# Performance work log

Measured on AMD Instinct MI355X. Metric: run time of the kernel, lower is better.

## Reference

```python
import jax, jax.numpy as jnp
import numpy as np

INPUT_SIZE, HIDDEN_SIZE, OUTPUT_SIZE, NUM_LAYERS = 64, 128, 32, 2
B, T = 256, 1024


def setup_inputs() -> dict:
    key = jax.random.key(0)
    ks = jax.random.split(key, 12)
    s = 1.0 / np.sqrt(HIDDEN_SIZE)  # PyTorch LSTM init range
    x = jax.random.normal(ks[0], (B, T, INPUT_SIZE), dtype=jnp.float32)
    h0 = jnp.zeros((NUM_LAYERS, B, HIDDEN_SIZE), dtype=jnp.float32)
    c0 = jnp.zeros((NUM_LAYERS, B, HIDDEN_SIZE), dtype=jnp.float32)
    # layer 0: input -> hidden; layer 1: hidden -> hidden. Gate order i,f,g,o (PyTorch).
    W_ih0 = jax.random.uniform(ks[1], (4 * HIDDEN_SIZE, INPUT_SIZE), minval=-s, maxval=s)
    W_hh0 = jax.random.uniform(ks[2], (4 * HIDDEN_SIZE, HIDDEN_SIZE), minval=-s, maxval=s)
    b_ih0 = jax.random.uniform(ks[3], (4 * HIDDEN_SIZE,), minval=-s, maxval=s)
    b_hh0 = jax.random.uniform(ks[4], (4 * HIDDEN_SIZE,), minval=-s, maxval=s)
    W_ih1 = jax.random.uniform(ks[5], (4 * HIDDEN_SIZE, HIDDEN_SIZE), minval=-s, maxval=s)
    W_hh1 = jax.random.uniform(ks[6], (4 * HIDDEN_SIZE, HIDDEN_SIZE), minval=-s, maxval=s)
    b_ih1 = jax.random.uniform(ks[7], (4 * HIDDEN_SIZE,), minval=-s, maxval=s)
    b_hh1 = jax.random.uniform(ks[8], (4 * HIDDEN_SIZE,), minval=-s, maxval=s)
    fc_w = jax.random.uniform(ks[9], (OUTPUT_SIZE, HIDDEN_SIZE), minval=-s, maxval=s)
    fc_b = jax.random.uniform(ks[10], (OUTPUT_SIZE,), minval=-s, maxval=s)
    return dict(x=x, h0=h0, c0=c0,
                W_ih0=W_ih0, W_hh0=W_hh0, b_ih0=b_ih0, b_hh0=b_hh0,
                W_ih1=W_ih1, W_hh1=W_hh1, b_ih1=b_ih1, b_hh1=b_hh1,
                fc_w=fc_w, fc_b=fc_b)


def _lstm_layer(x_btf, h0, c0, W_ih, W_hh, b_ih, b_hh):
    """x_btf: [B,T,F] -> (out [B,T,H], hT [B,H], cT [B,H]). PyTorch gate order i,f,g,o."""
    H = h0.shape[-1]
    # Precompute input contribution for all timesteps as one big GEMM.
    xp = jnp.einsum('btf,gf->btg', x_btf, W_ih) + b_ih + b_hh  # [B,T,4H]
    xp = jnp.swapaxes(xp, 0, 1)  # time-major [T,B,4H]

    def step(carry, xp_t):
        h, c = carry
        gates = xp_t + h @ W_hh.T  # [B,4H]
        i = jax.nn.sigmoid(gates[:, 0 * H:1 * H])
        f = jax.nn.sigmoid(gates[:, 1 * H:2 * H])
        g = jnp.tanh(gates[:, 2 * H:3 * H])
        o = jax.nn.sigmoid(gates[:, 3 * H:4 * H])
        c = f * c + i * g
        h = o * jnp.tanh(c)
        return (h, c), h

    (hT, cT), hs = jax.lax.scan(step, (h0, c0), xp)
    return jnp.swapaxes(hs, 0, 1), hT, cT  # back to batch_first


def reference(x, h0, c0, W_ih0, W_hh0, b_ih0, b_hh0,
              W_ih1, W_hh1, b_ih1, b_hh1, fc_w, fc_b):
    out0, h_0, c_0 = _lstm_layer(x, h0[0], c0[0], W_ih0, W_hh0, b_ih0, b_hh0)
    out1, h_1, c_1 = _lstm_layer(out0, h0[1], c0[1], W_ih1, W_hh1, b_ih1, b_hh1)
    out = jnp.einsum('bth,oh->bto', out1, fc_w) + fc_b  # [B,T,output_size]
    hN = jnp.stack([h_0, h_1])  # [num_layers,B,H]
    cN = jnp.stack([c_0, c_1])
    return out, hN, cN
```

## Files before the change

### kernel.cpp

```cpp
#include <hip/hip_runtime.h>


static constexpr int B   = 256;
static constexpr int T   = 1024;
static constexpr int H   = 128;
static constexpr int O   = 32;
static constexpr int R   = 4;
static constexpr int NBL = B / R;
static constexpr int CH  = 16;
static constexpr int NCH = T / CH;

typedef __attribute__((ext_vector_type(8))) short  short8;
typedef __attribute__((ext_vector_type(4))) float  f32x4;

#define LOG2E 1.4426950408889634f

#if __has_builtin(__builtin_amdgcn_exp2f)
#define EXP2(x) __builtin_amdgcn_exp2f(x)
#else
#define EXP2(x) __expf((x) * 0.69314718056f)
#endif
#if __has_builtin(__builtin_amdgcn_rcpf)
#define RCP(x) __builtin_amdgcn_rcpf(x)
#else
#define RCP(x) (1.0f / (x))
#endif

__device__ __forceinline__ unsigned short f2bf(float f) {
  unsigned int u = __builtin_bit_cast(unsigned int, f);
  u += 0x7fffu + ((u >> 16) & 1u);
  return (unsigned short)(u >> 16);
}

__device__ __forceinline__ float sigm(float x) {
  return RCP(1.0f + EXP2(-LOG2E * x));
}
__device__ __forceinline__ float tanh_f(float x) {
  return 1.0f - 2.0f * RCP(1.0f + EXP2(2.0f * LOG2E * x));
}

__device__ __forceinline__ void block_sync_lds() {
  __builtin_amdgcn_sched_barrier(0);
  asm volatile("s_waitcnt lgkmcnt(0)" ::: "memory");
  __builtin_amdgcn_s_barrier();
  __builtin_amdgcn_sched_barrier(0);
}

template <int KIN, bool IN_BF16, bool WRITE_HOUT, bool FUSE_FC, bool PROD, bool CONS>
__device__ __forceinline__ void scan_body(
    unsigned short* __restrict__ Ash,
    const void* __restrict__ in_,
    const float* __restrict__ h0,
    const float* __restrict__ c0,
    const float* __restrict__ Wih,
    const float* __restrict__ Whh,
    const float* __restrict__ bih,
    const float* __restrict__ bhh,
    unsigned short* __restrict__ hout,
    float* __restrict__ hN,
    float* __restrict__ cN,
    const float* __restrict__ Wfc,
    const float* __restrict__ bfc,
    float* __restrict__ fco,
    int* __restrict__ flag, const int bbase)
{
  constexpr int AK   = KIN + H;
  constexpr int KCX  = KIN / 32;
  constexpr int KCH  = H / 32;
  constexpr int APAD = AK + 8;

  const int tid  = threadIdx.x;
  const int w    = tid >> 6;
  const int l    = tid & 63;
  const int l15  = l & 15;
  const int lhi  = l >> 4;
  const int jcol = w * 16 + l15;

#define AEL(buf, row, col) Ash[(((buf) * 16 + (row)) * APAD) + (col)]

  short8 wfx[4][KCX], wfh[4][KCH];
  float  bias4[4];
#pragma unroll
  for (int gb = 0; gb < 4; ++gb) {
    const int gc = gb * H + jcol;
    const float* wi = Wih + (size_t)gc * KIN;
    const float* wh = Whh + (size_t)gc * H;
#pragma unroll
    for (int kc = 0; kc < KCX; ++kc) {
      const float* s = wi + kc * 32 + lhi * 8;
      float4 a = *(const float4*)s;
      float4 b = *(const float4*)(s + 4);
      short8 v;
      v[0] = (short)f2bf(a.x); v[1] = (short)f2bf(a.y);
      v[2] = (short)f2bf(a.z); v[3] = (short)f2bf(a.w);
      v[4] = (short)f2bf(b.x); v[5] = (short)f2bf(b.y);
      v[6] = (short)f2bf(b.z); v[7] = (short)f2bf(b.w);
      wfx[gb][kc] = v;
    }
#pragma unroll
    for (int kc = 0; kc < KCH; ++kc) {
      const float* s = wh + kc * 32 + lhi * 8;
      float4 a = *(const float4*)s;
      float4 b = *(const float4*)(s + 4);
      short8 v;
      v[0] = (short)f2bf(a.x); v[1] = (short)f2bf(a.y);
      v[2] = (short)f2bf(a.z); v[3] = (short)f2bf(a.w);
      v[4] = (short)f2bf(b.x); v[5] = (short)f2bf(b.y);
      v[6] = (short)f2bf(b.z); v[7] = (short)f2bf(b.w);
      wfh[gb][kc] = v;
    }
    bias4[gb] = bih[gc] + bhh[gc];
  }

  short8 bfr[4];
  float fcbias = 0.f;
  if constexpr (FUSE_FC) {
    const int oc = (w & 1) * 16 + l15;
#pragma unroll
    for (int kc = 0; kc < 4; ++kc) {
      const float* s = Wfc + (size_t)oc * H + kc * 32 + lhi * 8;
      float4 a = *(const float4*)s;
      float4 b = *(const float4*)(s + 4);
      short8 v;
      v[0] = (short)f2bf(a.x); v[1] = (short)f2bf(a.y);
      v[2] = (short)f2bf(a.z); v[3] = (short)f2bf(a.w);
      v[4] = (short)f2bf(b.x); v[5] = (short)f2bf(b.y);
      v[6] = (short)f2bf(b.z); v[7] = (short)f2bf(b.w);
      bfr[kc] = v;
    }
    fcbias = bfc[oc];
  }

  float cst   = c0[(size_t)(bbase + lhi) * H + jcol];
  float hlast = 0.f;

  const float*          inf = (const float*)in_;
  const unsigned short* inb = (const unsigned short*)in_;

  const bool sact = tid < 128;
  const int  srow = (tid >> 5) & 3;
  int scol;
  if constexpr (!IN_BF16) scol = (tid * 2) & 63;
  else                    scol = (tid * 4) & 127;
  const int srm = srow * 4;
  const float*          xpf = inf + (size_t)(bbase + srow) * T * KIN + scol;
  const unsigned short* xpb = inb + (size_t)(bbase + srow) * T * KIN + scol;

  unsigned short* hp = nullptr;
  if constexpr (WRITE_HOUT)
    hp = hout + (size_t)(bbase + lhi) * T * H + jcol;
  float* fp = nullptr;
  if constexpr (FUSE_FC)
    fp = fco + (size_t)(bbase + lhi) * T * O + (w & 1) * 16 + l15;

  for (int i = tid; i < 16 * APAD; i += 512)
    ((unsigned int*)Ash)[i] = 0u;
  __syncthreads();

  if constexpr (CONS) {
    if (tid == 0) {
      while (__hip_atomic_load(flag, __ATOMIC_ACQUIRE, __HIP_MEMORY_SCOPE_AGENT) < 2)
        __builtin_amdgcn_s_sleep(4);
    }
    __syncthreads();
  }

  if (sact) {
    if constexpr (!IN_BF16) {
      float2 v0 = *(const float2*)xpf;
      float2 v1 = *(const float2*)(xpf + KIN);
      *(unsigned int*)&AEL(1, srm, scol) =
          (unsigned int)f2bf(v0.x) | ((unsigned int)f2bf(v0.y) << 16);
      *(unsigned int*)&AEL(0, srm, scol) =
          (unsigned int)f2bf(v1.x) | ((unsigned int)f2bf(v1.y) << 16);
    } else {
      uint2 v0 = *(const uint2*)xpb;
      uint2 v1 = *(const uint2*)(xpb + KIN);
      *(uint2*)&AEL(1, srm, scol) = v0;
      *(uint2*)&AEL(0, srm, scol) = v1;
    }
  }
  if (tid < 128) {
    const int row = tid >> 5, col = (tid * 4) & 127;
    float4 v = *(const float4*)(h0 + (size_t)(bbase + row) * H + col);
    uint2 p;
    p.x = (unsigned int)f2bf(v.x) | ((unsigned int)f2bf(v.y) << 16);
    p.y = (unsigned int)f2bf(v.z) | ((unsigned int)f2bf(v.w) << 16);
    *(uint2*)&AEL(0, row * 4, KIN + col) = p;
  }

  float2 pfoF = {0.f, 0.f}; uint2 pfoB = {0u, 0u};
  if (sact) {
    if constexpr (!IN_BF16) pfoF = *(const float2*)(xpf + 2 * (size_t)KIN);
    else                    pfoB = *(const uint2*)(xpb + 2 * (size_t)KIN);
  }
  xpf += 3 * (size_t)KIN;
  xpb += 3 * (size_t)KIN;
  __syncthreads();

  f32x4 accX[4];
  {
    short8 afx[KCX];
#pragma unroll
    for (int kc = 0; kc < KCX; ++kc)
      afx[kc] = *(const short8*)&AEL(1, l15, kc * 32 + lhi * 8);
#pragma unroll
    for (int gb = 0; gb < 4; ++gb) {
      f32x4 a = {bias4[gb], bias4[gb], bias4[gb], bias4[gb]};
#pragma unroll
      for (int kc = 0; kc < KCX; ++kc)
        a = __builtin_amdgcn_mfma_f32_16x16x32_bf16(afx[kc], wfx[gb][kc], a, 0, 0, 0);
      accX[gb] = a;
    }
  }
  __syncthreads();

  int cur = 0;
  for (int k = 0; k < NCH; ++k) {
    if constexpr (CONS) {
      if (k > 0) {
        const int want = (k + 2 > NCH) ? NCH : (k + 2);
        if (tid == 0) {
          while (__hip_atomic_load(flag, __ATOMIC_ACQUIRE, __HIP_MEMORY_SCOPE_AGENT) < want)
            __builtin_amdgcn_s_sleep(4);
        }
        __syncthreads();
      }
    }

    for (int tt = 0; tt < CH; ++tt) {
      const int t   = k * CH + tt;
      const int nxt = cur ^ 1;

      float2 pfnF = {0.f, 0.f}; uint2 pfnB = {0u, 0u};
      if (sact) {
        if constexpr (!IN_BF16) {
          pfnF = *(const float2*)xpf;
          *(unsigned int*)&AEL(nxt, srm, scol) =
              (unsigned int)f2bf(pfoF.x) | ((unsigned int)f2bf(pfoF.y) << 16);
        } else {
          pfnB = *(const uint2*)xpb;
          *(uint2*)&AEL(nxt, srm, scol) = pfoB;
        }
      }

      short8 afh[KCH];
#pragma unroll
      for (int kc = 0; kc < KCH; ++kc)
        afh[kc] = *(const short8*)&AEL(cur, l15, KIN + kc * 32 + lhi * 8);
      short8 afx[KCX];
#pragma unroll
      for (int kc = 0; kc < KCX; ++kc)
        afx[kc] = *(const short8*)&AEL(cur, l15, kc * 32 + lhi * 8);

      f32x4 acc[4];
#pragma unroll
      for (int gb = 0; gb < 4; ++gb) {
        f32x4 a = accX[gb];
#pragma unroll
        for (int kc = 0; kc < KCH; ++kc)
          a = __builtin_amdgcn_mfma_f32_16x16x32_bf16(afh[kc], wfh[gb][kc], a, 0, 0, 0);
        acc[gb] = a;
      }

      f32x4 fs = {fcbias, fcbias, fcbias, fcbias};
      if constexpr (FUSE_FC) {
        if (w < 2 && t > 0) {
#pragma unroll
          for (int kc = 0; kc < 4; ++kc)
            fs = __builtin_amdgcn_mfma_f32_16x16x32_bf16(afh[kc], bfr[kc], fs, 0, 0, 0);
        }
      }

      {
        float i_ = sigm(acc[0][0]);
        float f_ = sigm(acc[1][0]);
        float g_ = tanh_f(acc[2][0]);
        float o_ = sigm(acc[3][0]);
        float c_ = f_ * cst + i_ * g_;
        cst = c_;
        float hn = o_ * tanh_f(c_);
        hlast = hn;
        unsigned short hb = f2bf(hn);
        AEL(nxt, lhi * 4, KIN + jcol) = hb;
        if constexpr (WRITE_HOUT) { hp[0] = hb; }
      }
      if constexpr (WRITE_HOUT) hp += H;

      if constexpr (FUSE_FC) {
        if (w < 2 && t > 0)
          fp[(size_t)(t - 1) * O] = fs[0];
      }

#pragma unroll
      for (int gb = 0; gb < 4; ++gb) {
        f32x4 a = {bias4[gb], bias4[gb], bias4[gb], bias4[gb]};
#pragma unroll
        for (int kc = 0; kc < KCX; ++kc)
          a = __builtin_amdgcn_mfma_f32_16x16x32_bf16(afx[kc], wfx[gb][kc], a, 0, 0, 0);
        accX[gb] = a;
      }

      block_sync_lds();
      cur = nxt;
      if constexpr (!IN_BF16) pfoF = pfnF; else pfoB = pfnB;
      if (t <= T - 5) { xpf += KIN; xpb += KIN; }
    }

    if constexpr (PROD) {
      __builtin_amdgcn_sched_barrier(0);
      asm volatile("s_waitcnt vmcnt(0)" ::: "memory");
      __builtin_amdgcn_s_barrier();
      if (tid == 0)
        __hip_atomic_store(flag, k + 1, __ATOMIC_RELEASE, __HIP_MEMORY_SCOPE_AGENT);
    }
  }

  {
    const size_t b = bbase + lhi;
    hN[b * H + jcol] = hlast;
    cN[b * H + jcol] = cst;
  }
  if constexpr (FUSE_FC) {
    if (w < 2) {
      short8 a4[4];
#pragma unroll
      for (int kc = 0; kc < 4; ++kc)
        a4[kc] = *(const short8*)&AEL(cur, l15, KIN + kc * 32 + lhi * 8);
      f32x4 fs = {fcbias, fcbias, fcbias, fcbias};
#pragma unroll
      for (int kc = 0; kc < 4; ++kc)
        fs = __builtin_amdgcn_mfma_f32_16x16x32_bf16(a4[kc], bfr[kc], fs, 0, 0, 0);
      fp[(size_t)(T - 1) * O] = fs[0];
    }
  }
#undef AEL
}

__global__ __launch_bounds__(512, 2) void lstm_fused(
    const float* __restrict__ x,
    const float* __restrict__ h0, const float* __restrict__ c0,
    const float* __restrict__ Wih0, const float* __restrict__ Whh0,
    const float* __restrict__ bih0, const float* __restrict__ bhh0,
    const float* __restrict__ Wih1, const float* __restrict__ Whh1,
    const float* __restrict__ bih1, const float* __restrict__ bhh1,
    const float* __restrict__ fcw, const float* __restrict__ fcb,
    unsigned short* __restrict__ out0,
    float* __restrict__ out, float* __restrict__ hN, float* __restrict__ cN,
    int* __restrict__ flags)
{
  __shared__ __align__(16) unsigned short Ash[2 * 16 * 264];
  const int bid = blockIdx.x;
  if (bid < NBL) {
    scan_body<64, false, true, false, true, false>(
        Ash, x, h0, c0, Wih0, Whh0, bih0, bhh0,
        out0, hN, cN, nullptr, nullptr, nullptr,
        flags + bid, bid * R);
  } else {
    const int rb = bid - NBL;
    scan_body<128, true, false, true, false, true>(
        Ash, out0, h0 + B * H, c0 + B * H, Wih1, Whh1, bih1, bhh1,
        nullptr, hN + B * H, cN + B * H, fcw, fcb, out,
        flags + rb, rb * R);
  }
}

extern "C" void kernel_launch(void* const* d_in, const int* in_sizes, int n_in,
                              void* d_out, int out_size, void* d_ws, size_t ws_size,
                              hipStream_t stream) {
  (void)in_sizes; (void)n_in; (void)out_size; (void)ws_size;

  const float* x    = (const float*)d_in[0];
  const float* h0   = (const float*)d_in[1];
  const float* c0   = (const float*)d_in[2];
  const float* Wih0 = (const float*)d_in[3];
  const float* Whh0 = (const float*)d_in[4];
  const float* bih0 = (const float*)d_in[5];
  const float* bhh0 = (const float*)d_in[6];
  const float* Wih1 = (const float*)d_in[7];
  const float* Whh1 = (const float*)d_in[8];
  const float* bih1 = (const float*)d_in[9];
  const float* bhh1 = (const float*)d_in[10];
  const float* fcw  = (const float*)d_in[11];
  const float* fcb  = (const float*)d_in[12];

  int*            flags = (int*)d_ws;
  unsigned short* out0  = (unsigned short*)((char*)d_ws + 1024);

  float* out = (float*)d_out;
  float* hN  = out + (size_t)B * T * O;
  float* cN  = hN + (size_t)2 * B * H;

  hipMemsetAsync(d_ws, 0, 1024, stream);
  lstm_fused<<<2 * NBL, 512, 0, stream>>>(
      x, h0, c0, Wih0, Whh0, bih0, bhh0, Wih1, Whh1, bih1, bhh1,
      fcw, fcb, out0, out, hN, cN, flags);
}
```

Measured before the change: 766.2 us.

## Load x operand fragments directly from global into registers, shrink LDS to h only

The per-step input rows no longer go through LDS. Each lane loads its MFMA A-fragment for x straight from global memory, two steps ahead; lanes that do not hold a real batch row read from a zeroed pad in the workspace. LDS now holds only the bf16 hidden state, stored in a pre-swizzled fragment layout so each lane reads it with one contiguous short8 per k-chunk. The x-projection MFMAs move earlier in the step, before the gate math. This removes LDS write/read traffic and bank-conflicted strided reads from the serial recurrence, at the cost of more global loads and registers per lane.

Measured after the change: 825.8 us. 1.08x slower.

```diff
diff --git a/kernel.cpp b/kernel.cpp
--- a/kernel.cpp
+++ b/kernel.cpp
@@ -62,12 +62,12 @@
     const float* __restrict__ Wfc,
     const float* __restrict__ bfc,
     float* __restrict__ fco,
+    const void* __restrict__ zpad,
     int* __restrict__ flag, const int bbase)
 {
-  constexpr int AK   = KIN + H;
   constexpr int KCX  = KIN / 32;
   constexpr int KCH  = H / 32;
-  constexpr int APAD = AK + 8;
+  constexpr int HBUF = KCH * 512;
 
   const int tid  = threadIdx.x;
   const int w    = tid >> 6;
@@ -75,8 +75,6 @@
   const int l15  = l & 15;
   const int lhi  = l >> 4;
   const int jcol = w * 16 + l15;
-
-#define AEL(buf, row, col) Ash[(((buf) * 16 + (row)) * APAD) + (col)]
 
   short8 wfx[4][KCX], wfh[4][KCH];
   float  bias4[4];
@@ -134,17 +132,23 @@
   float cst   = c0[(size_t)(bbase + lhi) * H + jcol];
   float hlast = 0.f;
 
-  const float*          inf = (const float*)in_;
-  const unsigned short* inb = (const unsigned short*)in_;
-
-  const bool sact = tid < 128;
-  const int  srow = (tid >> 5) & 3;
-  int scol;
-  if constexpr (!IN_BF16) scol = (tid * 2) & 63;
-  else                    scol = (tid * 4) & 127;
-  const int srm = srow * 4;
-  const float*          xpf = inf + (size_t)(bbase + srow) * T * KIN + scol;
-  const unsigned short* xpb = inb + (size_t)(bbase + srow) * T * KIN + scol;
+  const int hws = (jcol >> 5) * 512 +
+                  (lhi * 4 + 16 * ((w & 1) * 2 + (l15 >> 3))) * 8 + (jcol & 7);
+
+  const bool xact = (l15 & 3) == 0;
+  const int  br   = l15 >> 2;
+  const float*          xf = nullptr;
+  const unsigned short* xb = nullptr;
+  size_t xstep;
+  if constexpr (!IN_BF16) {
+    xf = xact ? ((const float*)in_ + (size_t)(bbase + br) * T * KIN + lhi * 8)
+              : (const float*)zpad;
+    xstep = xact ? (size_t)KIN : 0;
+  } else {
+    xb = xact ? ((const unsigned short*)in_ + (size_t)(bbase + br) * T * KIN + lhi * 8)
+              : (const unsigned short*)zpad;
+    xstep = xact ? (size_t)KIN : 0;
+  }
 
   unsigned short* hp = nullptr;
   if constexpr (WRITE_HOUT)
@@ -153,7 +157,7 @@
   if constexpr (FUSE_FC)
     fp = fco + (size_t)(bbase + lhi) * T * O + (w & 1) * 16 + l15;
 
-  for (int i = tid; i < 16 * APAD; i += 512)
+  for (int i = tid; i < HBUF; i += 512)
     ((unsigned int*)Ash)[i] = 0u;
   __syncthreads();
 
@@ -165,51 +169,57 @@
     __syncthreads();
   }
 
-  if (sact) {
-    if constexpr (!IN_BF16) {
-      float2 v0 = *(const float2*)xpf;
-      float2 v1 = *(const float2*)(xpf + KIN);
-      *(unsigned int*)&AEL(1, srm, scol) =
-          (unsigned int)f2bf(v0.x) | ((unsigned int)f2bf(v0.y) << 16);
-      *(unsigned int*)&AEL(0, srm, scol) =
-          (unsigned int)f2bf(v1.x) | ((unsigned int)f2bf(v1.y) << 16);
-    } else {
-      uint2 v0 = *(const uint2*)xpb;
-      uint2 v1 = *(const uint2*)(xpb + KIN);
-      *(uint2*)&AEL(1, srm, scol) = v0;
-      *(uint2*)&AEL(0, srm, scol) = v1;
-    }
-  }
-  if (tid < 128) {
-    const int row = tid >> 5, col = (tid * 4) & 127;
-    float4 v = *(const float4*)(h0 + (size_t)(bbase + row) * H + col);
-    uint2 p;
-    p.x = (unsigned int)f2bf(v.x) | ((unsigned int)f2bf(v.y) << 16);
-    p.y = (unsigned int)f2bf(v.z) | ((unsigned int)f2bf(v.w) << 16);
-    *(uint2*)&AEL(0, row * 4, KIN + col) = p;
-  }
-
-  float2 pfoF = {0.f, 0.f}; uint2 pfoB = {0u, 0u};
-  if (sact) {
-    if constexpr (!IN_BF16) pfoF = *(const float2*)(xpf + 2 * (size_t)KIN);
-    else                    pfoB = *(const uint2*)(xpb + 2 * (size_t)KIN);
-  }
-  xpf += 3 * (size_t)KIN;
-  xpb += 3 * (size_t)KIN;
-  __syncthreads();
+  Ash[hws] = f2bf(h0[(size_t)(bbase + lhi) * H + jcol]);
 
   f32x4 accX[4];
-  {
-    short8 afx[KCX];
-#pragma unroll
-    for (int kc = 0; kc < KCX; ++kc)
-      afx[kc] = *(const short8*)&AEL(1, l15, kc * 32 + lhi * 8);
+  float4 xcF[2 * KCX]; short8 xcB[KCX];
+  if constexpr (!IN_BF16) {
+    float4 x0[2 * KCX];
+#pragma unroll
+    for (int kc = 0; kc < KCX; ++kc) {
+      x0[2 * kc]     = *(const float4*)(xf + kc * 32);
+      x0[2 * kc + 1] = *(const float4*)(xf + kc * 32 + 4);
+    }
+    xf += xstep;
+#pragma unroll
+    for (int kc = 0; kc < KCX; ++kc) {
+      xcF[2 * kc]     = *(const float4*)(xf + kc * 32);
+      xcF[2 * kc + 1] = *(const float4*)(xf + kc * 32 + 4);
+    }
+    xf += xstep;
+    short8 fr[KCX];
+#pragma unroll
+    for (int kc = 0; kc < KCX; ++kc) {
+      float4 a = x0[2 * kc], b = x0[2 * kc + 1];
+      short8 v;
+      v[0] = (short)f2bf(a.x); v[1] = (short)f2bf(a.y);
+      v[2] = (short)f2bf(a.z); v[3] = (short)f2bf(a.w);
+      v[4] = (short)f2bf(b.x); v[5] = (short)f2bf(b.y);
+      v[6] = (short)f2bf(b.z); v[7] = (short)f2bf(b.w);
+      fr[kc] = v;
+    }
 #pragma unroll
     for (int gb = 0; gb < 4; ++gb) {
       f32x4 a = {bias4[gb], bias4[gb], bias4[gb], bias4[gb]};
 #pragma unroll
       for (int kc = 0; kc < KCX; ++kc)
-        a = __builtin_amdgcn_mfma_f32_16x16x32_bf16(afx[kc], wfx[gb][kc], a, 0, 0, 0);
+        a = __builtin_amdgcn_mfma_f32_16x16x32_bf16(fr[kc], wfx[gb][kc], a, 0, 0, 0);
+      accX[gb] = a;
+    }
+  } else {
+    short8 x0[KCX];
+#pragma unroll
+    for (int kc = 0; kc < KCX; ++kc) x0[kc] = *(const short8*)(xb + kc * 32);
+    xb += xstep;
+#pragma unroll
+    for (int kc = 0; kc < KCX; ++kc) xcB[kc] = *(const short8*)(xb + kc * 32);
+    xb += xstep;
+#pragma unroll
+    for (int gb = 0; gb < 4; ++gb) {
+      f32x4 a = {bias4[gb], bias4[gb], bias4[gb], bias4[gb]};
+#pragma unroll
+      for (int kc = 0; kc < KCX; ++kc)
+        a = __builtin_amdgcn_mfma_f32_16x16x32_bf16(x0[kc], wfx[gb][kc], a, 0, 0, 0);
       accX[gb] = a;
     }
   }
@@ -232,26 +242,22 @@
       const int t   = k * CH + tt;
       const int nxt = cur ^ 1;
 
-      float2 pfnF = {0.f, 0.f}; uint2 pfnB = {0u, 0u};
-      if (sact) {
-        if constexpr (!IN_BF16) {
-          pfnF = *(const float2*)xpf;
-          *(unsigned int*)&AEL(nxt, srm, scol) =
-              (unsigned int)f2bf(pfoF.x) | ((unsigned int)f2bf(pfoF.y) << 16);
-        } else {
-          pfnB = *(const uint2*)xpb;
-          *(uint2*)&AEL(nxt, srm, scol) = pfoB;
-        }
+      float4 xnF[2 * KCX]; short8 xnB[KCX];
+      if constexpr (!IN_BF16) {
+#pragma unroll
+        for (int kc = 0; kc < KCX; ++kc) {
+          xnF[2 * kc]     = *(const float4*)(xf + kc * 32);
+          xnF[2 * kc + 1] = *(const float4*)(xf + kc * 32 + 4);
+        }
+      } else {
+#pragma unroll
+        for (int kc = 0; kc < KCX; ++kc) xnB[kc] = *(const short8*)(xb + kc * 32);
       }
 
       short8 afh[KCH];
 #pragma unroll
       for (int kc = 0; kc < KCH; ++kc)
-        afh[kc] = *(const short8*)&AEL(cur, l15, KIN + kc * 32 + lhi * 8);
-      short8 afx[KCX];
-#pragma unroll
-      for (int kc = 0; kc < KCX; ++kc)
-        afx[kc] = *(const short8*)&AEL(cur, l15, kc * 32 + lhi * 8);
+        afh[kc] = *(const short8*)&Ash[cur * HBUF + kc * 512 + l * 8];
 
       f32x4 acc[4];
 #pragma unroll
@@ -269,6 +275,37 @@
 #pragma unroll
           for (int kc = 0; kc < 4; ++kc)
             fs = __builtin_amdgcn_mfma_f32_16x16x32_bf16(afh[kc], bfr[kc], fs, 0, 0, 0);
+        }
+      }
+
+      if constexpr (!IN_BF16) {
+        short8 fr[KCX];
+#pragma unroll
+        for (int kc = 0; kc < KCX; ++kc) {
+          float4 a = xcF[2 * kc], b = xcF[2 * kc + 1];
+          short8 v;
+          v[0] = (short)f2bf(a.x); v[1] = (short)f2bf(a.y);
+          v[2] = (short)f2bf(a.z); v[3] = (short)f2bf(a.w);
+          v[4] = (short)f2bf(b.x); v[5] = (short)f2bf(b.y);
+          v[6] = (short)f2bf(b.z); v[7] = (short)f2bf(b.w);
+          fr[kc] = v;
+        }
+#pragma unroll
+        for (int gb = 0; gb < 4; ++gb) {
+          f32x4 a = {bias4[gb], bias4[gb], bias4[gb], bias4[gb]};
+#pragma unroll
+          for (int kc = 0; kc < KCX; ++kc)
+            a = __builtin_amdgcn_mfma_f32_16x16x32_bf16(fr[kc], wfx[gb][kc], a, 0, 0, 0);
+          accX[gb] = a;
+        }
+      } else {
+#pragma unroll
+        for (int gb = 0; gb < 4; ++gb) {
+          f32x4 a = {bias4[gb], bias4[gb], bias4[gb], bias4[gb]};
+#pragma unroll
+          for (int kc = 0; kc < KCX; ++kc)
+            a = __builtin_amdgcn_mfma_f32_16x16x32_bf16(xcB[kc], wfx[gb][kc], a, 0, 0, 0);
+          accX[gb] = a;
         }
       }
 
@@ -282,7 +319,7 @@
         float hn = o_ * tanh_f(c_);
         hlast = hn;
         unsigned short hb = f2bf(hn);
-        AEL(nxt, lhi * 4, KIN + jcol) = hb;
+        Ash[nxt * HBUF + hws] = hb;
         if constexpr (WRITE_HOUT) { hp[0] = hb; }
       }
       if constexpr (WRITE_HOUT) hp += H;
@@ -292,19 +329,18 @@
           fp[(size_t)(t - 1) * O] = fs[0];
       }
 
-#pragma unroll
-      for (int gb = 0; gb < 4; ++gb) {
-        f32x4 a = {bias4[gb], bias4[gb], bias4[gb], bias4[gb]};
-#pragma unroll
-        for (int kc = 0; kc < KCX; ++kc)
-          a = __builtin_amdgcn_mfma_f32_16x16x32_bf16(afx[kc], wfx[gb][kc], a, 0, 0, 0);
-        accX[gb] = a;
+      if constexpr (!IN_BF16) {
+#pragma unroll
+        for (int q = 0; q < 2 * KCX; ++q) xcF[q] = xnF[q];
+        if (t <= T - 4) xf += xstep;
+      } else {
+#pragma unroll
+        for (int q = 0; q < KCX; ++q) xcB[q] = xnB[q];
+        if (t <= T - 4) xb += xstep;
       }
 
       block_sync_lds();
       cur = nxt;
-      if constexpr (!IN_BF16) pfoF = pfnF; else pfoB = pfnB;
-      if (t <= T - 5) { xpf += KIN; xpb += KIN; }
     }
 
     if constexpr (PROD) {
@@ -326,7 +362,7 @@
       short8 a4[4];
 #pragma unroll
       for (int kc = 0; kc < 4; ++kc)
-        a4[kc] = *(const short8*)&AEL(cur, l15, KIN + kc * 32 + lhi * 8);
+        a4[kc] = *(const short8*)&Ash[cur * HBUF + kc * 512 + l * 8];
       f32x4 fs = {fcbias, fcbias, fcbias, fcbias};
 #pragma unroll
       for (int kc = 0; kc < 4; ++kc)
@@ -334,7 +370,6 @@
       fp[(size_t)(T - 1) * O] = fs[0];
     }
   }
-#undef AEL
 }
 
 __global__ __launch_bounds__(512, 2) void lstm_fused(
@@ -347,20 +382,20 @@
     const float* __restrict__ fcw, const float* __restrict__ fcb,
     unsigned short* __restrict__ out0,
     float* __restrict__ out, float* __restrict__ hN, float* __restrict__ cN,
-    int* __restrict__ flags)
+    int* __restrict__ flags, const void* __restrict__ zpad)
 {
-  __shared__ __align__(16) unsigned short Ash[2 * 16 * 264];
+  __shared__ __align__(16) unsigned short Ash[2 * 2048];
   const int bid = blockIdx.x;
   if (bid < NBL) {
     scan_body<64, false, true, false, true, false>(
         Ash, x, h0, c0, Wih0, Whh0, bih0, bhh0,
-        out0, hN, cN, nullptr, nullptr, nullptr,
+        out0, hN, cN, nullptr, nullptr, nullptr, zpad,
         flags + bid, bid * R);
   } else {
     const int rb = bid - NBL;
     scan_body<128, true, false, true, false, true>(
         Ash, out0, h0 + B * H, c0 + B * H, Wih1, Whh1, bih1, bhh1,
-        nullptr, hN + B * H, cN + B * H, fcw, fcb, out,
+        nullptr, hN + B * H, cN + B * H, fcw, fcb, out, zpad,
         flags + rb, rb * R);
   }
 }
@@ -385,6 +420,7 @@
   const float* fcb  = (const float*)d_in[12];
 
   int*            flags = (int*)d_ws;
+  const void*     zpad  = (const void*)((char*)d_ws + 512);
   unsigned short* out0  = (unsigned short*)((char*)d_ws + 1024);
 
   float* out = (float*)d_out;
@@ -394,5 +430,5 @@
   hipMemsetAsync(d_ws, 0, 1024, stream);
   lstm_fused<<<2 * NBL, 512, 0, stream>>>(
       x, h0, c0, Wih0, Whh0, bih0, bhh0, Wih1, Whh1, bih1, bhh1,
-      fcw, fcb, out0, out, hN, cN, flags);
-}
+      fcw, fcb, out0, out, hN, cN, flags, zpad);
+}
```

## Batch input projection and FC per time chunk outside the recurrent loop

Applied to the files above, without the earlier changes.

The input-to-gate MFMA now runs once per chunk of 8 timesteps, packing 4 batch rows × 8 timesteps into full 16-row tiles. The results are stored to LDS as bf16 and read back at each step. The FC head is likewise computed once per chunk from buffered hidden states instead of per step, and the chunk size drops from 16 to 8. This takes the input GEMM and FC MFMAs off the serial per-step critical path and uses otherwise wasted tile rows, at the cost of more LDS traffic and bf16 rounding of the precomputed gate inputs.

After: 713.8 us. 6.8% less time.

```diff
diff --git a/kernel.cpp b/kernel.cpp
--- a/kernel.cpp
+++ b/kernel.cpp
@@ -7,8 +7,16 @@
 static constexpr int O   = 32;
 static constexpr int R   = 4;
 static constexpr int NBL = B / R;
-static constexpr int CH  = 16;
+static constexpr int CH  = 8;
 static constexpr int NCH = T / CH;
+
+static constexpr int HROW = H + 8;
+static constexpr int HB   = 0;
+static constexpr int HH   = HB + 2 * 16 * HROW;
+static constexpr int XB   = HH + 2 * 16 * HROW;
+static constexpr int AX   = XB + 2 * 16 * HROW;
+static constexpr int AXB  = 8 * 520 + 8;
+static constexpr int LDSN = AX + 4 * AXB;
 
 typedef __attribute__((ext_vector_type(8))) short  short8;
 typedef __attribute__((ext_vector_type(4))) float  f32x4;
@@ -31,6 +39,9 @@
   u += 0x7fffu + ((u >> 16) & 1u);
   return (unsigned short)(u >> 16);
 }
+__device__ __forceinline__ float bf2f(unsigned short s) {
+  return __builtin_bit_cast(float, (unsigned int)s << 16);
+}
 
 __device__ __forceinline__ float sigm(float x) {
   return RCP(1.0f + EXP2(-LOG2E * x));
@@ -48,7 +59,7 @@
 
 template <int KIN, bool IN_BF16, bool WRITE_HOUT, bool FUSE_FC, bool PROD, bool CONS>
 __device__ __forceinline__ void scan_body(
-    unsigned short* __restrict__ Ash,
+    unsigned short* __restrict__ S,
     const void* __restrict__ in_,
     const float* __restrict__ h0,
     const float* __restrict__ c0,
@@ -64,10 +75,9 @@
     float* __restrict__ fco,
     int* __restrict__ flag, const int bbase)
 {
-  constexpr int AK   = KIN + H;
   constexpr int KCX  = KIN / 32;
   constexpr int KCH  = H / 32;
-  constexpr int APAD = AK + 8;
+  constexpr int XROW = KIN + 8;
 
   const int tid  = threadIdx.x;
   const int w    = tid >> 6;
@@ -75,8 +85,6 @@
   const int l15  = l & 15;
   const int lhi  = l >> 4;
   const int jcol = w * 16 + l15;
-
-#define AEL(buf, row, col) Ash[(((buf) * 16 + (row)) * APAD) + (col)]
 
   short8 wfx[4][KCX], wfh[4][KCH];
   float  bias4[4];
@@ -137,24 +145,21 @@
   const float*          inf = (const float*)in_;
   const unsigned short* inb = (const unsigned short*)in_;
 
-  const bool sact = tid < 128;
-  const int  srow = (tid >> 5) & 3;
-  int scol;
-  if constexpr (!IN_BF16) scol = (tid * 2) & 63;
-  else                    scol = (tid * 4) & 127;
-  const int srm = srow * 4;
-  const float*          xpf = inf + (size_t)(bbase + srow) * T * KIN + scol;
-  const unsigned short* xpb = inb + (size_t)(bbase + srow) * T * KIN + scol;
+  const int sq  = tid >> 8;
+  const int srw = (tid >> 4) & 15;
+  const int sb  = bbase + sq * 2 + (srw >> 3);
+  const int sts = srw & 7;
+  const float*          xsf = inf + ((size_t)sb * T + sts) * KIN + (tid & 15) * 4;
+  const unsigned short* xsb = inb + ((size_t)sb * T + sts) * KIN + (tid & 15) * 8;
+  const int xdst = XB + (sq * 16 + srw) * XROW +
+                   (IN_BF16 ? (tid & 15) * 8 : (tid & 15) * 4);
 
   unsigned short* hp = nullptr;
   if constexpr (WRITE_HOUT)
     hp = hout + (size_t)(bbase + lhi) * T * H + jcol;
-  float* fp = nullptr;
-  if constexpr (FUSE_FC)
-    fp = fco + (size_t)(bbase + lhi) * T * O + (w & 1) * 16 + l15;
-
-  for (int i = tid; i < 16 * APAD; i += 512)
-    ((unsigned int*)Ash)[i] = 0u;
+
+  for (int i = tid; i < 2 * 16 * HROW / 2; i += 512)
+    ((unsigned int*)S)[i] = 0u;
   __syncthreads();
 
   if constexpr (CONS) {
@@ -165,54 +170,17 @@
     __syncthreads();
   }
 
-  if (sact) {
-    if constexpr (!IN_BF16) {
-      float2 v0 = *(const float2*)xpf;
-      float2 v1 = *(const float2*)(xpf + KIN);
-      *(unsigned int*)&AEL(1, srm, scol) =
-          (unsigned int)f2bf(v0.x) | ((unsigned int)f2bf(v0.y) << 16);
-      *(unsigned int*)&AEL(0, srm, scol) =
-          (unsigned int)f2bf(v1.x) | ((unsigned int)f2bf(v1.y) << 16);
-    } else {
-      uint2 v0 = *(const uint2*)xpb;
-      uint2 v1 = *(const uint2*)(xpb + KIN);
-      *(uint2*)&AEL(1, srm, scol) = v0;
-      *(uint2*)&AEL(0, srm, scol) = v1;
-    }
-  }
-  if (tid < 128) {
-    const int row = tid >> 5, col = (tid * 4) & 127;
-    float4 v = *(const float4*)(h0 + (size_t)(bbase + row) * H + col);
+  if constexpr (IN_BF16) {
+    uint4 v = *(const uint4*)xsb;
+    *(uint4*)&S[xdst] = v;
+  } else {
+    float4 v = *(const float4*)xsf;
     uint2 p;
     p.x = (unsigned int)f2bf(v.x) | ((unsigned int)f2bf(v.y) << 16);
     p.y = (unsigned int)f2bf(v.z) | ((unsigned int)f2bf(v.w) << 16);
-    *(uint2*)&AEL(0, row * 4, KIN + col) = p;
-  }
-
-  float2 pfoF = {0.f, 0.f}; uint2 pfoB = {0u, 0u};
-  if (sact) {
-    if constexpr (!IN_BF16) pfoF = *(const float2*)(xpf + 2 * (size_t)KIN);
-    else                    pfoB = *(const uint2*)(xpb + 2 * (size_t)KIN);
-  }
-  xpf += 3 * (size_t)KIN;
-  xpb += 3 * (size_t)KIN;
-  __syncthreads();
-
-  f32x4 accX[4];
-  {
-    short8 afx[KCX];
-#pragma unroll
-    for (int kc = 0; kc < KCX; ++kc)
-      afx[kc] = *(const short8*)&AEL(1, l15, kc * 32 + lhi * 8);
-#pragma unroll
-    for (int gb = 0; gb < 4; ++gb) {
-      f32x4 a = {bias4[gb], bias4[gb], bias4[gb], bias4[gb]};
-#pragma unroll
-      for (int kc = 0; kc < KCX; ++kc)
-        a = __builtin_amdgcn_mfma_f32_16x16x32_bf16(afx[kc], wfx[gb][kc], a, 0, 0, 0);
-      accX[gb] = a;
-    }
-  }
+    *(uint2*)&S[xdst] = p;
+  }
+  S[HB + (lhi * 4) * HROW + jcol] = f2bf(h0[(size_t)(bbase + lhi) * H + jcol]);
   __syncthreads();
 
   int cur = 0;
@@ -228,50 +196,66 @@
       }
     }
 
+#pragma unroll
+    for (int q = 0; q < 2; ++q) {
+      short8 afx[KCX];
+#pragma unroll
+      for (int kc = 0; kc < KCX; ++kc)
+        afx[kc] = *(const short8*)&S[XB + (q * 16 + l15) * XROW + kc * 32 + lhi * 8];
+#pragma unroll
+      for (int gb = 0; gb < 4; ++gb) {
+        f32x4 a = {bias4[gb], bias4[gb], bias4[gb], bias4[gb]};
+#pragma unroll
+        for (int kc = 0; kc < KCX; ++kc)
+          a = __builtin_amdgcn_mfma_f32_16x16x32_bf16(afx[kc], wfx[gb][kc], a, 0, 0, 0);
+        const int bb = q * 2 + (lhi >> 1);
+#pragma unroll
+        for (int r = 0; r < 4; ++r) {
+          const int ts = (lhi & 1) * 4 + r;
+          S[AX + bb * AXB + ts * 520 + gb * 128 + jcol] = f2bf(a[r]);
+        }
+      }
+    }
+
+    float4 sF; uint4 sB;
     for (int tt = 0; tt < CH; ++tt) {
-      const int t   = k * CH + tt;
-      const int nxt = cur ^ 1;
-
-      float2 pfnF = {0.f, 0.f}; uint2 pfnB = {0u, 0u};
-      if (sact) {
-        if constexpr (!IN_BF16) {
-          pfnF = *(const float2*)xpf;
-          *(unsigned int*)&AEL(nxt, srm, scol) =
-              (unsigned int)f2bf(pfoF.x) | ((unsigned int)f2bf(pfoF.y) << 16);
-        } else {
-          pfnB = *(const uint2*)xpb;
-          *(uint2*)&AEL(nxt, srm, scol) = pfoB;
+      if (k + 1 < NCH) {
+        if (tt == 0) {
+          if constexpr (IN_BF16) sB = *(const uint4*)(xsb + (size_t)(k + 1) * CH * KIN);
+          else                   sF = *(const float4*)(xsf + (size_t)(k + 1) * CH * KIN);
+        } else if (tt == 1) {
+          if constexpr (IN_BF16) {
+            *(uint4*)&S[xdst] = sB;
+          } else {
+            uint2 p;
+            p.x = (unsigned int)f2bf(sF.x) | ((unsigned int)f2bf(sF.y) << 16);
+            p.y = (unsigned int)f2bf(sF.z) | ((unsigned int)f2bf(sF.w) << 16);
+            *(uint2*)&S[xdst] = p;
+          }
         }
       }
 
+      float ax[4];
+#pragma unroll
+      for (int gb = 0; gb < 4; ++gb)
+        ax[gb] = bf2f(S[AX + lhi * AXB + tt * 520 + gb * 128 + jcol]);
+
       short8 afh[KCH];
 #pragma unroll
       for (int kc = 0; kc < KCH; ++kc)
-        afh[kc] = *(const short8*)&AEL(cur, l15, KIN + kc * 32 + lhi * 8);
-      short8 afx[KCX];
-#pragma unroll
-      for (int kc = 0; kc < KCX; ++kc)
-        afx[kc] = *(const short8*)&AEL(cur, l15, kc * 32 + lhi * 8);
+        afh[kc] = *(const short8*)&S[HB + (cur * 16 + l15) * HROW + kc * 32 + lhi * 8];
 
       f32x4 acc[4];
 #pragma unroll
       for (int gb = 0; gb < 4; ++gb) {
-        f32x4 a = accX[gb];
+        f32x4 a = {ax[gb], ax[gb], ax[gb], ax[gb]};
 #pragma unroll
         for (int kc = 0; kc < KCH; ++kc)
           a = __builtin_amdgcn_mfma_f32_16x16x32_bf16(afh[kc], wfh[gb][kc], a, 0, 0, 0);
         acc[gb] = a;
       }
 
-      f32x4 fs = {fcbias, fcbias, fcbias, fcbias};
-      if constexpr (FUSE_FC) {
-        if (w < 2 && t > 0) {
-#pragma unroll
-          for (int kc = 0; kc < 4; ++kc)
-            fs = __builtin_amdgcn_mfma_f32_16x16x32_bf16(afh[kc], bfr[kc], fs, 0, 0, 0);
-        }
-      }
-
+      const int nxt = cur ^ 1;
       {
         float i_ = sigm(acc[0][0]);
         float f_ = sigm(acc[1][0]);
@@ -282,29 +266,34 @@
         float hn = o_ * tanh_f(c_);
         hlast = hn;
         unsigned short hb = f2bf(hn);
-        AEL(nxt, lhi * 4, KIN + jcol) = hb;
+        S[HB + (nxt * 16 + lhi * 4) * HROW + jcol] = hb;
+        if constexpr (FUSE_FC)
+          S[HH + ((lhi >> 1) * 16 + (lhi & 1) * 8 + tt) * HROW + jcol] = hb;
         if constexpr (WRITE_HOUT) { hp[0] = hb; }
       }
       if constexpr (WRITE_HOUT) hp += H;
-
-      if constexpr (FUSE_FC) {
-        if (w < 2 && t > 0)
-          fp[(size_t)(t - 1) * O] = fs[0];
-      }
-
-#pragma unroll
-      for (int gb = 0; gb < 4; ++gb) {
-        f32x4 a = {bias4[gb], bias4[gb], bias4[gb], bias4[gb]};
-#pragma unroll
-        for (int kc = 0; kc < KCX; ++kc)
-          a = __builtin_amdgcn_mfma_f32_16x16x32_bf16(afx[kc], wfx[gb][kc], a, 0, 0, 0);
-        accX[gb] = a;
-      }
 
       block_sync_lds();
       cur = nxt;
-      if constexpr (!IN_BF16) pfoF = pfnF; else pfoB = pfnB;
-      if (t <= T - 5) { xpf += KIN; xpb += KIN; }
+    }
+
+    if constexpr (FUSE_FC) {
+      if (w < 4) {
+        const int q = w >> 1;
+        short8 a4[4];
+#pragma unroll
+        for (int kc = 0; kc < 4; ++kc)
+          a4[kc] = *(const short8*)&S[HH + (q * 16 + l15) * HROW + kc * 32 + lhi * 8];
+        f32x4 fs = {fcbias, fcbias, fcbias, fcbias};
+#pragma unroll
+        for (int kc = 0; kc < 4; ++kc)
+          fs = __builtin_amdgcn_mfma_f32_16x16x32_bf16(a4[kc], bfr[kc], fs, 0, 0, 0);
+        const int brow = bbase + q * 2 + (lhi >> 1);
+        const int tb   = k * CH + (lhi & 1) * 4;
+#pragma unroll
+        for (int r = 0; r < 4; ++r)
+          fco[((size_t)brow * T + tb + r) * O + (w & 1) * 16 + l15] = fs[r];
+      }
     }
 
     if constexpr (PROD) {
@@ -316,25 +305,8 @@
     }
   }
 
-  {
-    const size_t b = bbase + lhi;
-    hN[b * H + jcol] = hlast;
-    cN[b * H + jcol] = cst;
-  }
-  if constexpr (FUSE_FC) {
-    if (w < 2) {
-      short8 a4[4];
-#pragma unroll
-      for (int kc = 0; kc < 4; ++kc)
-        a4[kc] = *(const short8*)&AEL(cur, l15, KIN + kc * 32 + lhi * 8);
-      f32x4 fs = {fcbias, fcbias, fcbias, fcbias};
-#pragma unroll
-      for (int kc = 0; kc < 4; ++kc)
-        fs = __builtin_amdgcn_mfma_f32_16x16x32_bf16(a4[kc], bfr[kc], fs, 0, 0, 0);
-      fp[(size_t)(T - 1) * O] = fs[0];
-    }
-  }
-#undef AEL
+  hN[(size_t)(bbase + lhi) * H + jcol] = hlast;
+  cN[(size_t)(bbase + lhi) * H + jcol] = cst;
 }
 
 __global__ __launch_bounds__(512, 2) void lstm_fused(
@@ -349,17 +321,17 @@
     float* __restrict__ out, float* __restrict__ hN, float* __restrict__ cN,
     int* __restrict__ flags)
 {
-  __shared__ __align__(16) unsigned short Ash[2 * 16 * 264];
+  __shared__ __align__(16) unsigned short S[LDSN];
   const int bid = blockIdx.x;
   if (bid < NBL) {
     scan_body<64, false, true, false, true, false>(
-        Ash, x, h0, c0, Wih0, Whh0, bih0, bhh0,
+        S, x, h0, c0, Wih0, Whh0, bih0, bhh0,
         out0, hN, cN, nullptr, nullptr, nullptr,
         flags + bid, bid * R);
   } else {
     const int rb = bid - NBL;
     scan_body<128, true, false, true, false, true>(
-        Ash, out0, h0 + B * H, c0 + B * H, Wih1, Whh1, bih1, bhh1,
+        S, out0, h0 + B * H, c0 + B * H, Wih1, Whh1, bih1, bhh1,
         nullptr, hN + B * H, cN + B * H, fcw, fcb, out,
         flags + rb, rb * R);
   }
```
